# Performance work log

Hardware: AMD Instinct MI355X
Metric: run time of the kernel (lower is better)

## Reference

```python
import jax, jax.numpy as jnp
import numpy as np

B, S, D, H = 4, 2048, 1024, 16
DH = D // H  # 64


def setup_inputs() -> dict:
    key = jax.random.key(0)
    ks = jax.random.split(key, 7)
    scale = 1.0 / np.sqrt(DH)
    return {
        "elements": jax.random.normal(ks[0], (B, S, D), dtype=jnp.float32),
        # per-head Linear(d_head, d_head): weight [H, DH, DH] (out, in), bias [H, DH]
        "Wq": jax.random.normal(ks[1], (H, DH, DH), dtype=jnp.float32) * scale,
        "bq": jax.random.normal(ks[2], (H, DH), dtype=jnp.float32) * 0.01,
        "Wk": jax.random.normal(ks[3], (H, DH, DH), dtype=jnp.float32) * scale,
        "bk": jax.random.normal(ks[4], (H, DH), dtype=jnp.float32) * 0.01,
        "Wv": jax.random.normal(ks[5], (H, DH, DH), dtype=jnp.float32) * scale,
        "bv": jax.random.normal(ks[6], (H, DH), dtype=jnp.float32) * 0.01,
    }


def reference(elements, Wq, bq, Wk, bk, Wv, bv):
    b, s, d = elements.shape
    x = elements.reshape(b, s, H, DH)  # head-sliced channels
    # nn.Linear: y = x @ W.T + b, per head
    q = jnp.einsum("bshd,hed->bshe", x, Wq) + bq
    k = jnp.einsum("bshd,hed->bshe", x, Wk) + bk
    v = jnp.einsum("bshd,hed->bshe", x, Wv) + bv
    # NOTE: original scales by sqrt(nb_heads), not sqrt(d_head)
    scores = jnp.einsum("bshd,bthd->bhst", q, k) / jnp.sqrt(jnp.float32(H))
    attn = jax.nn.softmax(scores, axis=-1)
    out = jnp.einsum("bhst,bthd->bshd", attn, v)
    return out.reshape(b, s, d)
```

## Files before the change

kernel.cpp:

```cpp
#include <hip/hip_runtime.h>
#include <hip/hip_bf16.h>

#define BB 4
#define SS 2048
#define DD 1024
#define HH 16

typedef short bf16x8 __attribute__((ext_vector_type(8)));
typedef float f32x4 __attribute__((ext_vector_type(4)));
typedef float f32x16 __attribute__((ext_vector_type(16)));
typedef unsigned int uint32x4 __attribute__((ext_vector_type(4)));
typedef unsigned short u16x4 __attribute__((ext_vector_type(4)));

__device__ __forceinline__ unsigned short f2bf(float f) {
  __hip_bfloat16 h = __float2bfloat16(f);
  return __builtin_bit_cast(unsigned short, h);
}
__device__ __forceinline__ unsigned int pack2(float a, float b) {
  return (unsigned int)f2bf(a) | ((unsigned int)f2bf(b) << 16);
}
__device__ __forceinline__ void gl16(const unsigned short* g, unsigned short* l) {
  __builtin_amdgcn_global_load_lds(
      (const __attribute__((address_space(1))) void*)g,
      (__attribute__((address_space(3))) void*)l, 16, 0, 0);
}

__global__ __launch_bounds__(256) void qkv_proj(
    const float* __restrict__ x,
    const float* __restrict__ Wq, const float* __restrict__ bq,
    const float* __restrict__ Wk, const float* __restrict__ bk,
    const float* __restrict__ Wv, const float* __restrict__ bv,
    unsigned short* __restrict__ Q, unsigned short* __restrict__ K,
    unsigned short* __restrict__ Vt)
{
  __shared__ unsigned short Ql[64 * 64];
  __shared__ unsigned short Kl2[64 * 64];
  __shared__ unsigned short Vl2[64 * 64];

  const float QSC = 0.25f * 1.44269504088896f;
  int bid = blockIdx.x;
  int bh = bid & 63;
  int sbg = bid >> 6;
  int h = bh & (HH - 1);
  int b = bh >> 4;
  int t = threadIdx.x;
  int w = t >> 6, lane = t & 63;
  int g = lane >> 4, c = lane & 15;

  bf16x8 wqf[4][2], wkf[4][2], wvf[4][2];
#pragma unroll
  for (int et = 0; et < 4; ++et) {
#pragma unroll
    for (int kk = 0; kk < 2; ++kk) {
      int e = 16 * et + c;
      int d0 = 32 * kk + 8 * g;
      const float4* pq = reinterpret_cast<const float4*>(Wq + (h * 64 + e) * 64 + d0);
      const float4* pk = reinterpret_cast<const float4*>(Wk + (h * 64 + e) * 64 + d0);
      const float4* pv = reinterpret_cast<const float4*>(Wv + (h * 64 + e) * 64 + d0);
      float4 q0 = pq[0], q1 = pq[1];
      float4 k0 = pk[0], k1 = pk[1];
      float4 v0 = pv[0], v1 = pv[1];
      bf16x8 aq, ak, av;
      aq[0] = (short)f2bf(QSC * q0.x); aq[1] = (short)f2bf(QSC * q0.y);
      aq[2] = (short)f2bf(QSC * q0.z); aq[3] = (short)f2bf(QSC * q0.w);
      aq[4] = (short)f2bf(QSC * q1.x); aq[5] = (short)f2bf(QSC * q1.y);
      aq[6] = (short)f2bf(QSC * q1.z); aq[7] = (short)f2bf(QSC * q1.w);
      ak[0] = (short)f2bf(k0.x); ak[1] = (short)f2bf(k0.y);
      ak[2] = (short)f2bf(k0.z); ak[3] = (short)f2bf(k0.w);
      ak[4] = (short)f2bf(k1.x); ak[5] = (short)f2bf(k1.y);
      ak[6] = (short)f2bf(k1.z); ak[7] = (short)f2bf(k1.w);
      av[0] = (short)f2bf(v0.x); av[1] = (short)f2bf(v0.y);
      av[2] = (short)f2bf(v0.z); av[3] = (short)f2bf(v0.w);
      av[4] = (short)f2bf(v1.x); av[5] = (short)f2bf(v1.y);
      av[6] = (short)f2bf(v1.z); av[7] = (short)f2bf(v1.w);
      wqf[et][kk] = aq; wkf[et][kk] = ak; wvf[et][kk] = av;
    }
  }

  f32x4 bqv[4], bkv[4];
  float bvv[4];
#pragma unroll
  for (int et = 0; et < 4; ++et) {
#pragma unroll
    for (int r = 0; r < 4; ++r) {
      bqv[et][r] = QSC * bq[h * 64 + 16 * et + 4 * g + r];
      bkv[et][r] = bk[h * 64 + 16 * et + 4 * g + r];
    }
    bvv[et] = bv[h * 64 + 16 * et + c];
  }

  for (int i = 0; i < 4; ++i) {
    int sblk = (sbg * 4 + i) * 64;
    int s0 = sblk + w * 16;
    const float* xp = x + ((size_t)b * SS + s0 + c) * DD + h * 64;
    bf16x8 xf[2];
#pragma unroll
    for (int kk = 0; kk < 2; ++kk) {
      const float4* px = reinterpret_cast<const float4*>(xp + 32 * kk + 8 * g);
      float4 x0 = px[0], x1 = px[1];
      bf16x8 a;
      a[0] = (short)f2bf(x0.x); a[1] = (short)f2bf(x0.y);
      a[2] = (short)f2bf(x0.z); a[3] = (short)f2bf(x0.w);
      a[4] = (short)f2bf(x1.x); a[5] = (short)f2bf(x1.y);
      a[6] = (short)f2bf(x1.z); a[7] = (short)f2bf(x1.w);
      xf[kk] = a;
    }

    int sl = w * 16 + c;
#pragma unroll
    for (int et = 0; et < 4; ++et) {
      f32x4 aq = bqv[et];
      f32x4 ak = bkv[et];
      aq = __builtin_amdgcn_mfma_f32_16x16x32_bf16(wqf[et][0], xf[0], aq, 0, 0, 0);
      aq = __builtin_amdgcn_mfma_f32_16x16x32_bf16(wqf[et][1], xf[1], aq, 0, 0, 0);
      ak = __builtin_amdgcn_mfma_f32_16x16x32_bf16(wkf[et][0], xf[0], ak, 0, 0, 0);
      ak = __builtin_amdgcn_mfma_f32_16x16x32_bf16(wkf[et][1], xf[1], ak, 0, 0, 0);
      u16x4 pq, pk;
#pragma unroll
      for (int r = 0; r < 4; ++r) { pq[r] = f2bf(aq[r]); pk[r] = f2bf(ak[r]); }
      int g16 = 2 * et + (g >> 1), lo = g & 1;
      int off = sl * 64 + ((g16 ^ (sl & 7)) * 8) + lo * 4;
      *reinterpret_cast<u16x4*>(Ql + off) = pq;
      *reinterpret_cast<u16x4*>(Kl2 + off) = pk;
    }

#pragma unroll
    for (int et = 0; et < 4; ++et) {
      f32x4 av = {bvv[et], bvv[et], bvv[et], bvv[et]};
      av = __builtin_amdgcn_mfma_f32_16x16x32_bf16(xf[0], wvf[et][0], av, 0, 0, 0);
      av = __builtin_amdgcn_mfma_f32_16x16x32_bf16(xf[1], wvf[et][1], av, 0, 0, 0);
      u16x4 pv;
#pragma unroll
      for (int r = 0; r < 4; ++r) pv[r] = f2bf(av[r]);
      int re = 16 * et + c;
      int g16 = 2 * w + (g >> 1), lo = g & 1;
      int off = re * 64 + ((g16 ^ (re & 7)) * 8) + lo * 4;
      *reinterpret_cast<u16x4*>(Vl2 + off) = pv;
    }
    __syncthreads();

    size_t qkbase = ((size_t)bh * SS + sblk) * 64;
#pragma unroll
    for (int jj = 0; jj < 2; ++jj) {
      int idx = t + 256 * jj;
      int row = idx >> 3, g16 = idx & 7;
      int loff = row * 64 + ((g16 ^ (row & 7)) * 8);
      bf16x8 qv = *reinterpret_cast<const bf16x8*>(Ql + loff);
      bf16x8 kv = *reinterpret_cast<const bf16x8*>(Kl2 + loff);
      bf16x8 vv = *reinterpret_cast<const bf16x8*>(Vl2 + loff);
      *reinterpret_cast<bf16x8*>(Q + qkbase + (size_t)idx * 8) = qv;
      *reinterpret_cast<bf16x8*>(K + qkbase + (size_t)idx * 8) = kv;
      *reinterpret_cast<bf16x8*>(Vt + ((size_t)bh * 64 + row) * SS + sblk + g16 * 8) = vv;
    }
    __syncthreads();
  }
}

__global__ __launch_bounds__(256) void attn_fused(
    const unsigned short* __restrict__ Q, const unsigned short* __restrict__ K,
    const unsigned short* __restrict__ Vt, float* __restrict__ out)
{
  __shared__ unsigned short KLb[2][64 * 64];
  __shared__ unsigned short VLb[2][64 * 64];

  const int bid = blockIdx.x;
  const int bh = bid & 63;
  const int qblk = bid >> 6;
  const int t = threadIdx.x;
  const int w = t >> 6, lane = t & 63;
  const int c = lane & 31, hi = lane >> 5;
  const int lrow = lane >> 3, lg = lane & 7;

  const unsigned short* Qp = Q + ((size_t)bh * SS + qblk * 128 + w * 32 + c) * 64;
  bf16x8 qf[4];
#pragma unroll
  for (int ks = 0; ks < 4; ++ks)
    qf[ks] = *reinterpret_cast<const bf16x8*>(Qp + ks * 16 + 8 * hi);

  const unsigned short* Kp = K + (size_t)bh * SS * 64;
  const unsigned short* Vp = Vt + (size_t)bh * 64 * SS;

  f32x16 oacc[2];
#pragma unroll
  for (int dt = 0; dt < 2; ++dt)
#pragma unroll
    for (int r = 0; r < 16; ++r) oacc[dt][r] = 0.f;
  float lsum = 0.f;

#define STAGE(KV0, BUF)                                                        \
  {                                                                            \
    int kv0_ = (KV0);                                                          \
    _Pragma("unroll")                                                          \
    for (int i = 0; i < 2; ++i) {                                              \
      int row = w * 16 + i * 8 + lrow;                                         \
      int src = (lg ^ (row & 7) ^ (row >> 3)) & 7;                             \
      gl16(Kp + (size_t)(kv0_ + row) * 64 + src * 8,                           \
           &KLb[BUF][(w * 16 + i * 8) * 64]);                                  \
      gl16(Vp + (size_t)row * SS + kv0_ + src * 8,                             \
           &VLb[BUF][(w * 16 + i * 8) * 64]);                                  \
    }                                                                          \
  }

  STAGE(0, 0);
  __syncthreads();

  for (int t32 = 0; t32 < SS / 64; ++t32) {
    if (t32 + 1 < SS / 64) STAGE((t32 + 1) * 64, (t32 + 1) & 1);
    const unsigned short* Kl = KLb[t32 & 1];
    const unsigned short* Vl = VLb[t32 & 1];

    bf16x8 kfr[2][4];
#pragma unroll
    for (int st = 0; st < 2; ++st) {
      int row = st * 32 + c;
      int swz = ((row & 7) ^ (row >> 3)) & 7;
#pragma unroll
      for (int ks = 0; ks < 4; ++ks)
        kfr[st][ks] = *reinterpret_cast<const bf16x8*>(
            Kl + row * 64 + (((2 * ks + hi) ^ swz) & 7) * 8);
    }

    f32x16 sacc[2];
#pragma unroll
    for (int st = 0; st < 2; ++st)
#pragma unroll
      for (int r = 0; r < 16; ++r) sacc[st][r] = 0.f;
    __builtin_amdgcn_s_setprio(1);
#pragma unroll
    for (int st = 0; st < 2; ++st)
#pragma unroll
      for (int ks = 0; ks < 4; ++ks)
        sacc[st] = __builtin_amdgcn_mfma_f32_32x32x16_bf16(
            kfr[st][ks], qf[ks], sacc[st], 0, 0, 0);
    __builtin_amdgcn_s_setprio(0);

    bf16x8 vfr[2][4];
#pragma unroll
    for (int dt = 0; dt < 2; ++dt) {
      int row = dt * 32 + c;
      int swz = ((row & 7) ^ (row >> 3)) & 7;
#pragma unroll
      for (int ks = 0; ks < 4; ++ks)
        vfr[dt][ks] = *reinterpret_cast<const bf16x8*>(
            Vl + row * 64 + (((2 * ks + hi) ^ swz) & 7) * 8);
    }

    float psum = 0.f;
    unsigned int Wd[2][4][2];
#pragma unroll
    for (int st = 0; st < 2; ++st)
#pragma unroll
      for (int qd = 0; qd < 4; ++qd) {
        float p0 = __builtin_amdgcn_exp2f(sacc[st][4 * qd + 0]);
        float p1 = __builtin_amdgcn_exp2f(sacc[st][4 * qd + 1]);
        float p2 = __builtin_amdgcn_exp2f(sacc[st][4 * qd + 2]);
        float p3 = __builtin_amdgcn_exp2f(sacc[st][4 * qd + 3]);
        psum += (p0 + p1) + (p2 + p3);
        Wd[st][qd][0] = pack2(p0, p1);
        Wd[st][qd][1] = pack2(p2, p3);
      }
    psum += __shfl_xor(psum, 32);
    lsum += psum;

    bf16x8 pfrag[4];
#pragma unroll
    for (int ks = 0; ks < 4; ++ks) {
      int sti = ks >> 1, qd0 = 2 * (ks & 1);
      unsigned int s0 = hi ? Wd[sti][qd0][0] : Wd[sti][qd0 + 1][0];
      unsigned int s1 = hi ? Wd[sti][qd0][1] : Wd[sti][qd0 + 1][1];
      unsigned int r0 = (unsigned int)__shfl_xor((int)s0, 32);
      unsigned int r1 = (unsigned int)__shfl_xor((int)s1, 32);
      uint32x4 wv;
      wv[0] = hi ? r0 : Wd[sti][qd0][0];
      wv[1] = hi ? r1 : Wd[sti][qd0][1];
      wv[2] = hi ? Wd[sti][qd0 + 1][0] : r0;
      wv[3] = hi ? Wd[sti][qd0 + 1][1] : r1;
      pfrag[ks] = __builtin_bit_cast(bf16x8, wv);
    }

    __builtin_amdgcn_s_setprio(1);
#pragma unroll
    for (int dt = 0; dt < 2; ++dt)
#pragma unroll
      for (int ks = 0; ks < 4; ++ks)
        oacc[dt] = __builtin_amdgcn_mfma_f32_32x32x16_bf16(
            pfrag[ks], vfr[dt][ks], oacc[dt], 0, 0, 0);
    __builtin_amdgcn_s_setprio(0);

    __syncthreads();
  }

  const int b = bh >> 4, h = bh & (HH - 1);
  float* op = out + ((size_t)b * SS + qblk * 128 + w * 32) * DD + h * 64;
#pragma unroll
  for (int r = 0; r < 16; ++r) {
    int orow = (r & 3) + 8 * (r >> 2) + 4 * hi;
    float linv = 1.f / __shfl(lsum, orow);
    op[(size_t)orow * DD + c]      = oacc[0][r] * linv;
    op[(size_t)orow * DD + 32 + c] = oacc[1][r] * linv;
  }
}

extern "C" void kernel_launch(void* const* d_in, const int* in_sizes, int n_in,
                              void* d_out, int out_size, void* d_ws, size_t ws_size,
                              hipStream_t stream) {
  const float* x  = (const float*)d_in[0];
  const float* Wq = (const float*)d_in[1];
  const float* bq = (const float*)d_in[2];
  const float* Wk = (const float*)d_in[3];
  const float* bk = (const float*)d_in[4];
  const float* Wv = (const float*)d_in[5];
  const float* bv = (const float*)d_in[6];
  float* out = (float*)d_out;

  unsigned short* ws = (unsigned short*)d_ws;
  const size_t per = (size_t)BB * HH * SS * 64;
  unsigned short* Q  = ws;
  unsigned short* K  = ws + per;
  unsigned short* Vt = ws + 2 * per;

  qkv_proj<<<(BB * HH) * 8, 256, 0, stream>>>(x, Wq, bq, Wk, bk, Wv, bv, Q, K, Vt);
  attn_fused<<<(SS / 128) * (BB * HH), 256, 0, stream>>>(Q, K, Vt, out);
}
```

Measured before the change: 234.3 us.

## Stage K/V through registers and compute softmax row sums with MFMA

Replaces the double-buffered direct global-to-LDS loads with a single LDS buffer fed by register prefetch: the next K/V tile is loaded into registers while the current one is computed, then written to LDS at the top of the next iteration. The softmax denominator is now accumulated by an extra MFMA of the bf16 probabilities against a ones vector, replacing the float adds and cross-lane shuffles. This frees LDS and VALU/shuffle work but adds MFMA work, one extra barrier-ordered LDS write per tile, and sums the bf16-rounded probabilities rather than the fp32 ones.

```diff
diff --git a/kernel.cpp b/kernel.cpp
--- a/kernel.cpp
+++ b/kernel.cpp
@@ -18,11 +18,6 @@
 }
 __device__ __forceinline__ unsigned int pack2(float a, float b) {
   return (unsigned int)f2bf(a) | ((unsigned int)f2bf(b) << 16);
-}
-__device__ __forceinline__ void gl16(const unsigned short* g, unsigned short* l) {
-  __builtin_amdgcn_global_load_lds(
-      (const __attribute__((address_space(1))) void*)g,
-      (__attribute__((address_space(3))) void*)l, 16, 0, 0);
 }
 
 __global__ __launch_bounds__(256) void qkv_proj(
@@ -160,8 +155,8 @@
     const unsigned short* __restrict__ Q, const unsigned short* __restrict__ K,
     const unsigned short* __restrict__ Vt, float* __restrict__ out)
 {
-  __shared__ unsigned short KLb[2][64 * 64];
-  __shared__ unsigned short VLb[2][64 * 64];
+  __shared__ unsigned short Kl[64 * 64];
+  __shared__ unsigned short Vl[64 * 64];
 
   const int bid = blockIdx.x;
   const int bh = bid & 63;
@@ -169,7 +164,6 @@
   const int t = threadIdx.x;
   const int w = t >> 6, lane = t & 63;
   const int c = lane & 31, hi = lane >> 5;
-  const int lrow = lane >> 3, lg = lane & 7;
 
   const unsigned short* Qp = Q + ((size_t)bh * SS + qblk * 128 + w * 32 + c) * 64;
   bf16x8 qf[4];
@@ -180,59 +174,72 @@
   const unsigned short* Kp = K + (size_t)bh * SS * 64;
   const unsigned short* Vp = Vt + (size_t)bh * 64 * SS;
 
-  f32x16 oacc[2];
+  bf16x8 ones;
+#pragma unroll
+  for (int j = 0; j < 8; ++j) ones[j] = (short)0x3F80;
+
+  f32x16 oacc[2], lacc;
 #pragma unroll
   for (int dt = 0; dt < 2; ++dt)
 #pragma unroll
     for (int r = 0; r < 16; ++r) oacc[dt][r] = 0.f;
-  float lsum = 0.f;
-
-#define STAGE(KV0, BUF)                                                        \
-  {                                                                            \
-    int kv0_ = (KV0);                                                          \
-    _Pragma("unroll")                                                          \
-    for (int i = 0; i < 2; ++i) {                                              \
-      int row = w * 16 + i * 8 + lrow;                                         \
-      int src = (lg ^ (row & 7) ^ (row >> 3)) & 7;                             \
-      gl16(Kp + (size_t)(kv0_ + row) * 64 + src * 8,                           \
-           &KLb[BUF][(w * 16 + i * 8) * 64]);                                  \
-      gl16(Vp + (size_t)row * SS + kv0_ + src * 8,                             \
-           &VLb[BUF][(w * 16 + i * 8) * 64]);                                  \
-    }                                                                          \
-  }
-
-  STAGE(0, 0);
-  __syncthreads();
-
-  for (int t32 = 0; t32 < SS / 64; ++t32) {
-    if (t32 + 1 < SS / 64) STAGE((t32 + 1) * 64, (t32 + 1) & 1);
-    const unsigned short* Kl = KLb[t32 & 1];
-    const unsigned short* Vl = VLb[t32 & 1];
-
-    bf16x8 kfr[2][4];
+#pragma unroll
+  for (int r = 0; r < 16; ++r) lacc[r] = 0.f;
+
+  int srow[2], sdst[2], ssrc[2];
+#pragma unroll
+  for (int i = 0; i < 2; ++i) {
+    int ci = t + 256 * i;
+    int row = ci >> 3, seg = ci & 7;
+    int gsw = (seg ^ (row & 7) ^ (row >> 3)) & 7;
+    srow[i] = row; sdst[i] = row * 64 + gsw * 8; ssrc[i] = seg * 8;
+  }
+
+  bf16x8 kreg[2], vreg[2];
+#pragma unroll
+  for (int i = 0; i < 2; ++i) {
+    kreg[i] = *reinterpret_cast<const bf16x8*>(Kp + (size_t)srow[i] * 64 + ssrc[i]);
+    vreg[i] = *reinterpret_cast<const bf16x8*>(Vp + (size_t)srow[i] * SS + ssrc[i]);
+  }
+
+  for (int kv0 = 0; kv0 < SS; kv0 += 64) {
+#pragma unroll
+    for (int i = 0; i < 2; ++i) {
+      *reinterpret_cast<bf16x8*>(Kl + sdst[i]) = kreg[i];
+      *reinterpret_cast<bf16x8*>(Vl + sdst[i]) = vreg[i];
+    }
+    __syncthreads();
+
+    if (kv0 + 64 < SS) {
+#pragma unroll
+      for (int i = 0; i < 2; ++i) {
+        kreg[i] = *reinterpret_cast<const bf16x8*>(
+            Kp + (size_t)(kv0 + 64 + srow[i]) * 64 + ssrc[i]);
+        vreg[i] = *reinterpret_cast<const bf16x8*>(
+            Vp + (size_t)srow[i] * SS + kv0 + 64 + ssrc[i]);
+      }
+    }
+
+    f32x16 sacc[2];
+#pragma unroll
+    for (int st = 0; st < 2; ++st)
+#pragma unroll
+      for (int r = 0; r < 16; ++r) sacc[st][r] = 0.f;
 #pragma unroll
     for (int st = 0; st < 2; ++st) {
       int row = st * 32 + c;
       int swz = ((row & 7) ^ (row >> 3)) & 7;
+      bf16x8 kf[4];
 #pragma unroll
       for (int ks = 0; ks < 4; ++ks)
-        kfr[st][ks] = *reinterpret_cast<const bf16x8*>(
+        kf[ks] = *reinterpret_cast<const bf16x8*>(
             Kl + row * 64 + (((2 * ks + hi) ^ swz) & 7) * 8);
-    }
-
-    f32x16 sacc[2];
-#pragma unroll
-    for (int st = 0; st < 2; ++st)
-#pragma unroll
-      for (int r = 0; r < 16; ++r) sacc[st][r] = 0.f;
-    __builtin_amdgcn_s_setprio(1);
-#pragma unroll
-    for (int st = 0; st < 2; ++st)
+      __builtin_amdgcn_s_setprio(1);
 #pragma unroll
       for (int ks = 0; ks < 4; ++ks)
-        sacc[st] = __builtin_amdgcn_mfma_f32_32x32x16_bf16(
-            kfr[st][ks], qf[ks], sacc[st], 0, 0, 0);
-    __builtin_amdgcn_s_setprio(0);
+        sacc[st] = __builtin_amdgcn_mfma_f32_32x32x16_bf16(kf[ks], qf[ks], sacc[st], 0, 0, 0);
+      __builtin_amdgcn_s_setprio(0);
+    }
 
     bf16x8 vfr[2][4];
 #pragma unroll
@@ -245,7 +252,6 @@
             Vl + row * 64 + (((2 * ks + hi) ^ swz) & 7) * 8);
     }
 
-    float psum = 0.f;
     unsigned int Wd[2][4][2];
 #pragma unroll
     for (int st = 0; st < 2; ++st)
@@ -255,12 +261,9 @@
         float p1 = __builtin_amdgcn_exp2f(sacc[st][4 * qd + 1]);
         float p2 = __builtin_amdgcn_exp2f(sacc[st][4 * qd + 2]);
         float p3 = __builtin_amdgcn_exp2f(sacc[st][4 * qd + 3]);
-        psum += (p0 + p1) + (p2 + p3);
         Wd[st][qd][0] = pack2(p0, p1);
         Wd[st][qd][1] = pack2(p2, p3);
       }
-    psum += __shfl_xor(psum, 32);
-    lsum += psum;
 
     bf16x8 pfrag[4];
 #pragma unroll
@@ -280,6 +283,9 @@
 
     __builtin_amdgcn_s_setprio(1);
 #pragma unroll
+    for (int ks = 0; ks < 4; ++ks)
+      lacc = __builtin_amdgcn_mfma_f32_32x32x16_bf16(pfrag[ks], ones, lacc, 0, 0, 0);
+#pragma unroll
     for (int dt = 0; dt < 2; ++dt)
 #pragma unroll
       for (int ks = 0; ks < 4; ++ks)
@@ -295,7 +301,7 @@
 #pragma unroll
   for (int r = 0; r < 16; ++r) {
     int orow = (r & 3) + 8 * (r >> 2) + 4 * hi;
-    float linv = 1.f / __shfl(lsum, orow);
+    float linv = 1.f / lacc[r];
     op[(size_t)orow * DD + c]      = oacc[0][r] * linv;
     op[(size_t)orow * DD + 32 + c] = oacc[1][r] * linv;
   }
```

Measured after the change: 219.9 us. 6.1% less time.
